# Performance work log

Measured on AMD Instinct MI355X. Metric: run time of the kernel, lower is better.

## Reference

```python
import jax, jax.numpy as jnp
import numpy as np

B, N, DIM, HEADS, DIM_HEAD = 1, 8192, 512, 8, 64  # dim == heads*dim_head required by pos_emb
EPS = 1e-12  # F.normalize eps


def setup_inputs() -> dict:
    key = jax.random.key(0)
    ks = jax.random.split(key, 13)
    w = lambda k, shape: jax.random.normal(k, shape, dtype=jnp.float32) * 0.02
    return {
        "x_in": jax.random.normal(ks[0], (B, N, DIM), dtype=jnp.float32),
        "task_x": jax.random.normal(ks[1], (B, N, DIM), dtype=jnp.float32),
        "Ges": jax.random.uniform(ks[2], (1, 1, N, N), dtype=jnp.float32) / N,  # OT transport plan (precomputed constant)
        "Wq": w(ks[3], (DIM, DIM)),
        "Wk": w(ks[4], (DIM, DIM)),
        "Wv": w(ks[5], (DIM, DIM)),
        "rescale": jnp.ones((HEADS, 1, 1), dtype=jnp.float32),
        "Wp": w(ks[6], (DIM, DIM)),
        "bp": jnp.zeros((DIM,), dtype=jnp.float32),
        "W1": w(ks[7], (DIM, DIM)),
        "b1": jnp.zeros((DIM,), dtype=jnp.float32),
        "W2": w(ks[8], (DIM, DIM)),
        "b2": jnp.zeros((DIM,), dtype=jnp.float32),
    }


def _l2norm(x):
    # F.normalize(p=2, dim=-1): x / max(||x||, eps)
    n = jnp.sqrt(jnp.sum(x * x, axis=-1, keepdims=True))
    return x / jnp.maximum(n, EPS)


def reference(x_in, task_x, Ges, Wq, Wk, Wv, rescale, Wp, bp, W1, b1, W2, b2):
    b, n, c = x_in.shape
    q_inp = x_in @ Wq.T          # [b,n,hd]
    k_inp = x_in @ Wk.T
    v_inp = x_in @ Wv.T
    split = lambda t: t.reshape(b, n, HEADS, DIM_HEAD).transpose(0, 2, 1, 3)  # [b,h,n,d]
    q, k, v, tx = split(q_inp), split(k_inp), split(v_inp), split(task_x)
    guided = (Ges @ tx) * v       # [b,h,n,d]: OT-guided embedding multiply
    # channel attention: operate along n, attend over d
    qT = _l2norm(q.transpose(0, 1, 3, 2))   # [b,h,d,n]
    kT = _l2norm(k.transpose(0, 1, 3, 2))   # [b,h,d,n]
    gT = guided.transpose(0, 1, 3, 2)        # [b,h,d,n]
    attn = jnp.einsum('bhdn,bhen->bhde', kT, qT) * rescale  # [b,h,d,d]
    attn = jax.nn.softmax(attn, axis=-1)
    x = attn @ gT                 # [b,h,d,n]
    x = x.transpose(0, 3, 1, 2).reshape(b, n, HEADS * DIM_HEAD)  # [b,n,hd]
    out_c = x @ Wp.T + bp
    out_p = (jax.nn.gelu(v_inp @ W1.T + b1, approximate=False)) @ W2.T + b2
    return out_c + out_p
```

## Files before the change

kernel.cpp:

```cpp
#include <hip/hip_runtime.h>
#include <hip/hip_bf16.h>

typedef unsigned short u16;
typedef __attribute__((ext_vector_type(8))) short short8v;
typedef __attribute__((ext_vector_type(4))) float f32x4;

typedef __attribute__((address_space(3))) char lds_char;
typedef const __attribute__((address_space(1))) char g_char;

__device__ __forceinline__ u16 f2bf(float f) {
    union { float f; unsigned int u; } x; x.f = f;
    unsigned int u = x.u;
    return (u16)((u + 0x7FFFu + ((u >> 16) & 1u)) >> 16);
}
__device__ __forceinline__ float bf2f(u16 h) {
    union { unsigned int u; float f; } x; x.u = ((unsigned int)h) << 16;
    return x.f;
}
__device__ __forceinline__ u16 cvtbf(float f) {
    return __builtin_bit_cast(u16, __float2bfloat16(f));
}
__device__ __forceinline__ void gload16(const void* g, void* l) {
    __builtin_amdgcn_global_load_lds((g_char*)g, (lds_char*)l, 16, 0, 0);
}

template<int EPI, bool AF32>
__global__ __launch_bounds__(256, 3) void gemm_k(
    const void* __restrict__ Ap, int lda,
    const u16* __restrict__ Bt, int ldb,
    void* __restrict__ Cp, int ldc, int K)
{
    constexpr int ATB = AF32 ? 32768 : 16384;
    __shared__ alignas(16) char smem[ATB + 16384];

    const int t     = threadIdx.x;
    const int lane  = t & 63;
    const int wid   = t >> 6;
    const int m0    = blockIdx.x * 128;
    const int n0    = blockIdx.y * 128;
    const int kbase = blockIdx.z * K;
    const int wr    = wid >> 1, wc = wid & 1;
    const int lr    = lane & 15, q4 = lane >> 4;

    f32x4 acc[4][4];
    #pragma unroll
    for (int i = 0; i < 4; ++i)
        #pragma unroll
        for (int j = 0; j < 4; ++j)
            acc[i][j] = (f32x4){0.f, 0.f, 0.f, 0.f};

    const int nsteps = K >> 6;
    for (int kt = 0; kt < nsteps; ++kt) {
        const int k0 = kbase + (kt << 6);
        if constexpr (AF32) {
            const float* A32 = (const float*)Ap;
            #pragma unroll
            for (int p = 0; p < 8; ++p) {
                int o   = p * 4096 + t * 16;
                int row = o >> 8;
                int cb  = (o & 255) ^ ((row & 15) << 4);
                gload16(A32 + (size_t)(m0 + row) * (size_t)lda + k0 + (cb >> 2),
                        smem + o);
            }
        } else {
            const u16* A16 = (const u16*)Ap;
            #pragma unroll
            for (int p = 0; p < 4; ++p) {
                int o   = p * 4096 + t * 16;
                int row = o >> 7;
                int cb  = (o & 127) ^ ((row & 7) << 4);
                gload16(A16 + (size_t)(m0 + row) * (size_t)lda + k0 + (cb >> 1),
                        smem + o);
            }
        }
        #pragma unroll
        for (int p = 0; p < 4; ++p) {
            int o   = p * 4096 + t * 16;
            int row = o >> 7;
            int cb  = (o & 127) ^ ((row & 7) << 4);
            gload16(Bt + (size_t)(n0 + row) * (size_t)ldb + k0 + (cb >> 1),
                    smem + ATB + o);
        }
        __syncthreads();

        #pragma unroll
        for (int kh = 0; kh < 2; ++kh) {
            short8v a[4], b[4];
            #pragma unroll
            for (int i = 0; i < 4; ++i) {
                int ar = wr * 64 + i * 16 + lr;
                if constexpr (AF32) {
                    int cb0 = kh * 128 + q4 * 32;
                    int sw  = (ar & 15) << 4;
                    f32x4 f0 = *(const f32x4*)(smem + ar * 256 + (cb0 ^ sw));
                    f32x4 f1 = *(const f32x4*)(smem + ar * 256 + ((cb0 + 16) ^ sw));
                    short8v av;
                    #pragma unroll
                    for (int j = 0; j < 4; ++j) {
                        av[j]     = (short)cvtbf(f0[j]);
                        av[j + 4] = (short)cvtbf(f1[j]);
                    }
                    a[i] = av;
                } else {
                    a[i] = *(const short8v*)(smem + ar * 128 +
                            ((kh * 64 + q4 * 16) ^ ((ar & 7) << 4)));
                }
            }
            #pragma unroll
            for (int i = 0; i < 4; ++i) {
                int br = wc * 64 + i * 16 + lr;
                b[i] = *(const short8v*)(smem + ATB + br * 128 +
                        ((kh * 64 + q4 * 16) ^ ((br & 7) << 4)));
            }
            #pragma unroll
            for (int mi = 0; mi < 4; ++mi)
                #pragma unroll
                for (int ni = 0; ni < 4; ++ni)
                    acc[mi][ni] = __builtin_amdgcn_mfma_f32_16x16x32_bf16(
                        a[mi], b[ni], acc[mi][ni], 0, 0, 0);
        }
        __syncthreads();
    }

    const size_t zoff = (size_t)blockIdx.z * 8192ull * (size_t)ldc;
    #pragma unroll
    for (int mi = 0; mi < 4; ++mi) {
        #pragma unroll
        for (int ni = 0; ni < 4; ++ni) {
            const int gc = n0 + wc * 64 + ni * 16 + lr;
            #pragma unroll
            for (int j = 0; j < 4; ++j) {
                const int gr = m0 + wr * 64 + mi * 16 + q4 * 4 + j;
                float v = acc[mi][ni][j];
                if constexpr (EPI == 0) {
                    ((u16*)Cp)[(size_t)gr * ldc + gc] = f2bf(v);
                } else {
                    ((float*)Cp)[zoff + (size_t)gr * ldc + gc] = v;
                }
            }
        }
    }
}

template<int KZ, int MODE>
__global__ void k_cmb(const float* __restrict__ P, const u16* __restrict__ QKV,
                      const float* __restrict__ bvec, void* __restrict__ dst)
{
    for (int i = blockIdx.x * 256 + threadIdx.x; i < 1048576;
         i += gridDim.x * 256) {
        const int r = i >> 7, c = (i & 127) * 4;
        f32x4 s = ((const f32x4*)P)[i];
        #pragma unroll
        for (int z = 1; z < KZ; ++z) {
            f32x4 q = ((const f32x4*)P)[(size_t)z * 1048576 + i];
            s[0] += q[0]; s[1] += q[1]; s[2] += q[2]; s[3] += q[3];
        }
        if constexpr (MODE == 1) {
            ushort4 v = *(const ushort4*)(QKV + (size_t)r * 1536 + 1024 + c);
            ushort4 o;
            o.x = cvtbf(s[0] * bf2f(v.x)); o.y = cvtbf(s[1] * bf2f(v.y));
            o.z = cvtbf(s[2] * bf2f(v.z)); o.w = cvtbf(s[3] * bf2f(v.w));
            *(ushort4*)((u16*)dst + (size_t)r * 1024 + c) = o;
        } else if constexpr (MODE == 2) {
            float4 b = *(const float4*)(bvec + c);
            float x0 = s[0] + b.x, x1 = s[1] + b.y, x2 = s[2] + b.z, x3 = s[3] + b.w;
            ushort4 o;
            o.x = cvtbf(0.5f * x0 * (1.0f + erff(x0 * 0.70710678118f)));
            o.y = cvtbf(0.5f * x1 * (1.0f + erff(x1 * 0.70710678118f)));
            o.z = cvtbf(0.5f * x2 * (1.0f + erff(x2 * 0.70710678118f)));
            o.w = cvtbf(0.5f * x3 * (1.0f + erff(x3 * 0.70710678118f)));
            *(ushort4*)((u16*)dst + (size_t)r * 1024 + 512 + c) = o;
        } else {
            float4 b = *(const float4*)(bvec + c);
            float4 o = {s[0] + b.x, s[1] + b.y, s[2] + b.z, s[3] + b.w};
            *(float4*)((float*)dst + (size_t)r * 512 + c) = o;
        }
    }
}

__global__ void k_convert(const float* __restrict__ Wq, const float* __restrict__ Wk,
                          const float* __restrict__ Wv, const float* __restrict__ W1,
                          u16* __restrict__ WqkvB, u16* __restrict__ W1B)
{
    const int C2 = 196608;
    const int C3 = 65536;
    for (int i = blockIdx.x * blockDim.x + threadIdx.x; i < C2 + C3;
         i += gridDim.x * blockDim.x) {
        const float* src; u16* dst;
        if (i < C2) {
            int e = i * 4;
            if (e < 262144)      src = Wq + e;
            else if (e < 524288) src = Wk + (e - 262144);
            else                 src = Wv + (e - 524288);
            dst = WqkvB + e;
        } else {
            int e = (i - C2) * 4;
            src = W1 + e; dst = W1B + e;
        }
        float4 v = *reinterpret_cast<const float4*>(src);
        ushort4 h;
        h.x = f2bf(v.x); h.y = f2bf(v.y); h.z = f2bf(v.z); h.w = f2bf(v.w);
        *reinterpret_cast<ushort4*>(dst) = h;
    }
}

__global__ void k_transpose(const float* __restrict__ tx, u16* __restrict__ txt)
{
    __shared__ float tile[64][65];
    const int n0 = blockIdx.x * 64;
    const int c0 = blockIdx.y * 64;
    const int t = threadIdx.x;
    #pragma unroll
    for (int p = 0; p < 4; ++p) {
        int q = p * 256 + t;
        int r = q >> 4, s = q & 15;
        float4 v = *reinterpret_cast<const float4*>(tx + (size_t)(n0 + r) * 512 + c0 + s * 4);
        tile[r][s * 4 + 0] = v.x; tile[r][s * 4 + 1] = v.y;
        tile[r][s * 4 + 2] = v.z; tile[r][s * 4 + 3] = v.w;
    }
    __syncthreads();
    #pragma unroll
    for (int p = 0; p < 4; ++p) {
        int q = p * 256 + t;
        int cc = q >> 4, s = q & 15;
        ushort4 h;
        h.x = f2bf(tile[s * 4 + 0][cc]); h.y = f2bf(tile[s * 4 + 1][cc]);
        h.z = f2bf(tile[s * 4 + 2][cc]); h.w = f2bf(tile[s * 4 + 3][cc]);
        *reinterpret_cast<ushort4*>(txt + (size_t)(c0 + cc) * 8192 + n0 + s * 4) = h;
    }
}

__global__ void k_colsq(const u16* __restrict__ QKV, float* __restrict__ colsq)
{
    const int t = threadIdx.x;
    const int c8 = t & 127, rs = t >> 7;
    float a[8];
    #pragma unroll
    for (int j = 0; j < 8; ++j) a[j] = 0.f;
    const int row0 = blockIdx.x * 64;
    for (int rr = rs; rr < 64; rr += 2) {
        uint4 u = *reinterpret_cast<const uint4*>(QKV + (size_t)(row0 + rr) * 1536 + c8 * 8);
        unsigned int w[4] = {u.x, u.y, u.z, u.w};
        #pragma unroll
        for (int q = 0; q < 4; ++q) {
            float f0 = bf2f((u16)(w[q] & 0xffffu));
            float f1 = bf2f((u16)(w[q] >> 16));
            a[2 * q]     += f0 * f0;
            a[2 * q + 1] += f1 * f1;
        }
    }
    #pragma unroll
    for (int j = 0; j < 8; ++j) atomicAdd(&colsq[c8 * 8 + j], a[j]);
}

__global__ void k_gram(const u16* __restrict__ QKV, float* __restrict__ Sb)
{
    __shared__ u16 Qt[4][64];
    __shared__ u16 Kt[4][64];
    const int h = blockIdx.x >> 6;
    const int chunk = blockIdx.x & 63;
    const int t = threadIdx.x;
    const int e = t & 63;
    const int dg = t >> 6;
    float acc[16];
    #pragma unroll
    for (int k = 0; k < 16; ++k) acc[k] = 0.f;
    const int rowbase = chunk * 128;
    for (int p = 0; p < 32; ++p) {
        __syncthreads();
        if (t < 64) {
            const int mat = t >> 5, sub = t & 31, r = sub >> 3, seg = sub & 7;
            const int row = rowbase + p * 4 + r;
            const int col = (mat ? 512 : 0) + h * 64 + seg * 8;
            uint4 v = *reinterpret_cast<const uint4*>(QKV + (size_t)row * 1536 + col);
            u16* dst = mat ? &Kt[r][seg * 8] : &Qt[r][seg * 8];
            *reinterpret_cast<uint4*>(dst) = v;
        }
        __syncthreads();
        #pragma unroll
        for (int r = 0; r < 4; ++r) {
            const float q = bf2f(Qt[r][e]);
            short8v kv0 = *reinterpret_cast<const short8v*>(&Kt[r][dg * 16]);
            short8v kv1 = *reinterpret_cast<const short8v*>(&Kt[r][dg * 16 + 8]);
            #pragma unroll
            for (int k = 0; k < 8; ++k) {
                acc[k]     += bf2f((u16)kv0[k]) * q;
                acc[k + 8] += bf2f((u16)kv1[k]) * q;
            }
        }
    }
    #pragma unroll
    for (int k = 0; k < 16; ++k)
        atomicAdd(&Sb[h * 4096 + (dg * 16 + k) * 64 + e], acc[k]);
}

__global__ void k_softmax(const float* __restrict__ Sb, const float* __restrict__ colsq,
                          const float* __restrict__ rescale, float* __restrict__ Abuf)
{
    const int h = blockIdx.x;
    const int t = threadIdx.x;
    const float rsc = rescale[h];
    const float nq = fmaxf(sqrtf(colsq[h * 64 + t]), 1e-12f);
    for (int d = 0; d < 64; ++d) {
        const float nk = fmaxf(sqrtf(colsq[512 + h * 64 + d]), 1e-12f);
        float v = Sb[h * 4096 + d * 64 + t] / (nk * nq) * rsc;
        float m = v;
        #pragma unroll
        for (int off = 32; off > 0; off >>= 1) m = fmaxf(m, __shfl_xor(m, off, 64));
        float p = expf(v - m);
        float s = p;
        #pragma unroll
        for (int off = 32; off > 0; off >>= 1) s += __shfl_xor(s, off, 64);
        Abuf[h * 4096 + d * 64 + t] = p / s;
    }
}

__global__ void k_buildbt(const float* __restrict__ Abuf, const float* __restrict__ Wp,
                          const float* __restrict__ W2, const float* __restrict__ bp,
                          const float* __restrict__ b2, u16* __restrict__ BtC,
                          float* __restrict__ bsum)
{
    const int g = blockIdx.x * 256 + threadIdx.x;
    const int j = g >> 10, c = g & 1023;
    if (c < 512) {
        const int h = c >> 6, e = c & 63;
        const float* Ah = Abuf + h * 4096 + e;
        const float* Wph = Wp + (size_t)j * 512 + h * 64;
        float s = 0.f;
        #pragma unroll 8
        for (int d = 0; d < 64; ++d) s += Ah[d * 64] * Wph[d];
        BtC[(size_t)j * 1024 + c] = f2bf(s);
        if (c == 0) bsum[j] = bp[j] + b2[j];
    } else {
        BtC[(size_t)j * 1024 + c] = f2bf(W2[(size_t)j * 512 + (c - 512)]);
    }
}

extern "C" void kernel_launch(void* const* d_in, const int* in_sizes, int n_in,
                              void* d_out, int out_size, void* d_ws, size_t ws_size,
                              hipStream_t stream)
{
    const float* x_in    = (const float*)d_in[0];
    const float* task_x  = (const float*)d_in[1];
    const float* Ges     = (const float*)d_in[2];
    const float* Wq      = (const float*)d_in[3];
    const float* Wk      = (const float*)d_in[4];
    const float* Wv      = (const float*)d_in[5];
    const float* rescale = (const float*)d_in[6];
    const float* Wp      = (const float*)d_in[7];
    const float* bp      = (const float*)d_in[8];
    const float* W1      = (const float*)d_in[9];
    const float* b1      = (const float*)d_in[10];
    const float* W2      = (const float*)d_in[11];
    const float* b2      = (const float*)d_in[12];
    float* out = (float*)d_out;
    char* ws = (char*)d_ws;

    u16*   TXT   = (u16*)  (ws + 0);
    u16*   QKV   = (u16*)  (ws + 8388608);
    u16*   AH    = (u16*)  (ws + 33554432);
    u16*   WqkvB = (u16*)  (ws + 50331648);
    u16*   W1B   = (u16*)  (ws + 51904512);
    u16*   BtC   = (u16*)  (ws + 52428800);
    float* colsq = (float*)(ws + 53477376);
    float* Sb    = (float*)(ws + 53481472);
    float* Abuf  = (float*)(ws + 53612544);
    float* bsum  = (float*)(ws + 53743616);
    float* P     = (float*)(ws + 53745664);
    (void)in_sizes; (void)n_in; (void)out_size; (void)ws_size;

    hipMemsetAsync(colsq, 0, 135168, stream);

    k_convert  <<<512, 256, 0, stream>>>(Wq, Wk, Wv, W1, WqkvB, W1B);
    k_transpose<<<dim3(128, 8), 256, 0, stream>>>(task_x, TXT);

    gemm_k<0, true><<<dim3(64, 12, 1), 256, 0, stream>>>(
        x_in, 512, WqkvB, 512, QKV, 1536, 512);

    k_colsq  <<<128, 256, 0, stream>>>(QKV, colsq);
    k_gram   <<<512, 256, 0, stream>>>(QKV, Sb);
    k_softmax<<<8, 64, 0, stream>>>(Sb, colsq, rescale, Abuf);
    k_buildbt<<<2048, 256, 0, stream>>>(Abuf, Wp, W2, bp, b2, BtC, bsum);

    gemm_k<4, true><<<dim3(64, 4, 4), 256, 0, stream>>>(
        Ges, 8192, TXT, 8192, P, 512, 2048);
    k_cmb<4, 1><<<1024, 256, 0, stream>>>(P, QKV, nullptr, AH);

    gemm_k<4, false><<<dim3(64, 4, 2), 256, 0, stream>>>(
        QKV + 1024, 1536, W1B, 512, P, 512, 256);
    k_cmb<2, 2><<<1024, 256, 0, stream>>>(P, nullptr, b1, AH);

    gemm_k<4, false><<<dim3(64, 4, 2), 256, 0, stream>>>(
        AH, 1024, BtC, 1024, P, 512, 512);
    k_cmb<2, 3><<<1024, 256, 0, stream>>>(P, nullptr, bsum, out);
}
```

Baseline: 369.7 us.

## Convert fp32 A tiles to bf16 before LDS store; widen gram staging tile

In the GEMM, fp32 A tiles are now loaded into registers, converted to bf16 once and written to LDS. The old path staged fp32 through async global-to-LDS loads and converted on every fragment read. This halves the A tile's LDS footprint (allowing better occupancy) and removes repeated conversions, at the cost of synchronous register-staged loads that no longer bypass VGPRs. In the gram kernel, each iteration now stages 16 rows with all threads instead of 4 rows with 64 threads, cutting the number of barriers per block.

```diff
diff --git a/kernel.cpp b/kernel.cpp
--- a/kernel.cpp
+++ b/kernel.cpp
@@ -30,8 +30,7 @@
     const u16* __restrict__ Bt, int ldb,
     void* __restrict__ Cp, int ldc, int K)
 {
-    constexpr int ATB = AF32 ? 32768 : 16384;
-    __shared__ alignas(16) char smem[ATB + 16384];
+    __shared__ alignas(16) char smem[32768];
 
     const int t     = threadIdx.x;
     const int lane  = t & 63;
@@ -52,15 +51,18 @@
     const int nsteps = K >> 6;
     for (int kt = 0; kt < nsteps; ++kt) {
         const int k0 = kbase + (kt << 6);
+
+        float4 ar[8];
         if constexpr (AF32) {
             const float* A32 = (const float*)Ap;
             #pragma unroll
-            for (int p = 0; p < 8; ++p) {
+            for (int p = 0; p < 4; ++p) {
                 int o   = p * 4096 + t * 16;
-                int row = o >> 8;
-                int cb  = (o & 255) ^ ((row & 15) << 4);
-                gload16(A32 + (size_t)(m0 + row) * (size_t)lda + k0 + (cb >> 2),
-                        smem + o);
+                int row = o >> 7;
+                int fc  = (o & 127) >> 1;
+                const float* gp = A32 + (size_t)(m0 + row) * (size_t)lda + k0 + fc;
+                ar[2 * p]     = *(const float4*)gp;
+                ar[2 * p + 1] = *(const float4*)(gp + 4);
             }
         } else {
             const u16* A16 = (const u16*)Ap;
@@ -79,7 +81,23 @@
             int row = o >> 7;
             int cb  = (o & 127) ^ ((row & 7) << 4);
             gload16(Bt + (size_t)(n0 + row) * (size_t)ldb + k0 + (cb >> 1),
-                    smem + ATB + o);
+                    smem + 16384 + o);
+        }
+        if constexpr (AF32) {
+            #pragma unroll
+            for (int p = 0; p < 4; ++p) {
+                int o   = p * 4096 + t * 16;
+                int row = o >> 7;
+                int cb  = o & 127;
+                const float* f0 = (const float*)&ar[2 * p];
+                const float* f1 = (const float*)&ar[2 * p + 1];
+                uint4 w;
+                w.x = (unsigned)cvtbf(f0[0]) | ((unsigned)cvtbf(f0[1]) << 16);
+                w.y = (unsigned)cvtbf(f0[2]) | ((unsigned)cvtbf(f0[3]) << 16);
+                w.z = (unsigned)cvtbf(f1[0]) | ((unsigned)cvtbf(f1[1]) << 16);
+                w.w = (unsigned)cvtbf(f1[2]) | ((unsigned)cvtbf(f1[3]) << 16);
+                *(uint4*)(smem + row * 128 + (cb ^ ((row & 7) << 4))) = w;
+            }
         }
         __syncthreads();
 
@@ -88,28 +106,14 @@
             short8v a[4], b[4];
             #pragma unroll
             for (int i = 0; i < 4; ++i) {
-                int ar = wr * 64 + i * 16 + lr;
-                if constexpr (AF32) {
-                    int cb0 = kh * 128 + q4 * 32;
-                    int sw  = (ar & 15) << 4;
-                    f32x4 f0 = *(const f32x4*)(smem + ar * 256 + (cb0 ^ sw));
-                    f32x4 f1 = *(const f32x4*)(smem + ar * 256 + ((cb0 + 16) ^ sw));
-                    short8v av;
-                    #pragma unroll
-                    for (int j = 0; j < 4; ++j) {
-                        av[j]     = (short)cvtbf(f0[j]);
-                        av[j + 4] = (short)cvtbf(f1[j]);
-                    }
-                    a[i] = av;
-                } else {
-                    a[i] = *(const short8v*)(smem + ar * 128 +
-                            ((kh * 64 + q4 * 16) ^ ((ar & 7) << 4)));
-                }
+                int arr = wr * 64 + i * 16 + lr;
+                a[i] = *(const short8v*)(smem + arr * 128 +
+                        ((kh * 64 + q4 * 16) ^ ((arr & 7) << 4)));
             }
             #pragma unroll
             for (int i = 0; i < 4; ++i) {
                 int br = wc * 64 + i * 16 + lr;
-                b[i] = *(const short8v*)(smem + ATB + br * 128 +
+                b[i] = *(const short8v*)(smem + 16384 + br * 128 +
                         ((kh * 64 + q4 * 16) ^ ((br & 7) << 4)));
             }
             #pragma unroll
@@ -255,8 +259,8 @@
 
 __global__ void k_gram(const u16* __restrict__ QKV, float* __restrict__ Sb)
 {
-    __shared__ u16 Qt[4][64];
-    __shared__ u16 Kt[4][64];
+    __shared__ u16 Qt[16][64];
+    __shared__ u16 Kt[16][64];
     const int h = blockIdx.x >> 6;
     const int chunk = blockIdx.x & 63;
     const int t = threadIdx.x;
@@ -266,11 +270,11 @@
     #pragma unroll
     for (int k = 0; k < 16; ++k) acc[k] = 0.f;
     const int rowbase = chunk * 128;
-    for (int p = 0; p < 32; ++p) {
+    for (int p = 0; p < 8; ++p) {
         __syncthreads();
-        if (t < 64) {
-            const int mat = t >> 5, sub = t & 31, r = sub >> 3, seg = sub & 7;
-            const int row = rowbase + p * 4 + r;
+        {
+            const int mat = t >> 7, sub = t & 127, r = sub >> 3, seg = sub & 7;
+            const int row = rowbase + p * 16 + r;
             const int col = (mat ? 512 : 0) + h * 64 + seg * 8;
             uint4 v = *reinterpret_cast<const uint4*>(QKV + (size_t)row * 1536 + col);
             u16* dst = mat ? &Kt[r][seg * 8] : &Qt[r][seg * 8];
@@ -278,7 +282,7 @@
         }
         __syncthreads();
         #pragma unroll
-        for (int r = 0; r < 4; ++r) {
+        for (int r = 0; r < 16; ++r) {
             const float q = bf2f(Qt[r][e]);
             short8v kv0 = *reinterpret_cast<const short8v*>(&Kt[r][dg * 16]);
             short8v kv1 = *reinterpret_cast<const short8v*>(&Kt[r][dg * 16 + 8]);
```

Result: slower. 429.3 us (+16.1%).

## Pre-convert Ges and x_in to bf16 and simplify GEMM to bf16-only A

Applied to the files above, without the earlier changes.

Adds a standalone kernel that converts the large Ges matrix to bf16 and extends the weight-conversion kernel to also convert x_in. The GEMM kernel drops its fp32-A path, halving its LDS footprint and raising the occupancy hint. This removes per-tile fp32 loads and in-loop conversions. In exchange, it adds an extra full pass writing and then re-reading a bf16 copy of Ges each call.

```diff
diff --git a/kernel.cpp b/kernel.cpp
--- a/kernel.cpp
+++ b/kernel.cpp
@@ -24,14 +24,13 @@
     __builtin_amdgcn_global_load_lds((g_char*)g, (lds_char*)l, 16, 0, 0);
 }
 
-template<int EPI, bool AF32>
-__global__ __launch_bounds__(256, 3) void gemm_k(
-    const void* __restrict__ Ap, int lda,
+template<int EPI>
+__global__ __launch_bounds__(256, 4) void gemm_k(
+    const u16* __restrict__ Ab, int lda,
     const u16* __restrict__ Bt, int ldb,
     void* __restrict__ Cp, int ldc, int K)
 {
-    constexpr int ATB = AF32 ? 32768 : 16384;
-    __shared__ alignas(16) char smem[ATB + 16384];
+    __shared__ alignas(16) char smem[32768];
 
     const int t     = threadIdx.x;
     const int lane  = t & 63;
@@ -52,26 +51,13 @@
     const int nsteps = K >> 6;
     for (int kt = 0; kt < nsteps; ++kt) {
         const int k0 = kbase + (kt << 6);
-        if constexpr (AF32) {
-            const float* A32 = (const float*)Ap;
-            #pragma unroll
-            for (int p = 0; p < 8; ++p) {
-                int o   = p * 4096 + t * 16;
-                int row = o >> 8;
-                int cb  = (o & 255) ^ ((row & 15) << 4);
-                gload16(A32 + (size_t)(m0 + row) * (size_t)lda + k0 + (cb >> 2),
-                        smem + o);
-            }
-        } else {
-            const u16* A16 = (const u16*)Ap;
-            #pragma unroll
-            for (int p = 0; p < 4; ++p) {
-                int o   = p * 4096 + t * 16;
-                int row = o >> 7;
-                int cb  = (o & 127) ^ ((row & 7) << 4);
-                gload16(A16 + (size_t)(m0 + row) * (size_t)lda + k0 + (cb >> 1),
-                        smem + o);
-            }
+        #pragma unroll
+        for (int p = 0; p < 4; ++p) {
+            int o   = p * 4096 + t * 16;
+            int row = o >> 7;
+            int cb  = (o & 127) ^ ((row & 7) << 4);
+            gload16(Ab + (size_t)(m0 + row) * (size_t)lda + k0 + (cb >> 1),
+                    smem + o);
         }
         #pragma unroll
         for (int p = 0; p < 4; ++p) {
@@ -79,7 +65,7 @@
             int row = o >> 7;
             int cb  = (o & 127) ^ ((row & 7) << 4);
             gload16(Bt + (size_t)(n0 + row) * (size_t)ldb + k0 + (cb >> 1),
-                    smem + ATB + o);
+                    smem + 16384 + o);
         }
         __syncthreads();
 
@@ -89,27 +75,13 @@
             #pragma unroll
             for (int i = 0; i < 4; ++i) {
                 int ar = wr * 64 + i * 16 + lr;
-                if constexpr (AF32) {
-                    int cb0 = kh * 128 + q4 * 32;
-                    int sw  = (ar & 15) << 4;
-                    f32x4 f0 = *(const f32x4*)(smem + ar * 256 + (cb0 ^ sw));
-                    f32x4 f1 = *(const f32x4*)(smem + ar * 256 + ((cb0 + 16) ^ sw));
-                    short8v av;
-                    #pragma unroll
-                    for (int j = 0; j < 4; ++j) {
-                        av[j]     = (short)cvtbf(f0[j]);
-                        av[j + 4] = (short)cvtbf(f1[j]);
-                    }
-                    a[i] = av;
-                } else {
-                    a[i] = *(const short8v*)(smem + ar * 128 +
-                            ((kh * 64 + q4 * 16) ^ ((ar & 7) << 4)));
-                }
+                a[i] = *(const short8v*)(smem + ar * 128 +
+                        ((kh * 64 + q4 * 16) ^ ((ar & 7) << 4)));
             }
             #pragma unroll
             for (int i = 0; i < 4; ++i) {
                 int br = wc * 64 + i * 16 + lr;
-                b[i] = *(const short8v*)(smem + ATB + br * 128 +
+                b[i] = *(const short8v*)(smem + 16384 + br * 128 +
                         ((kh * 64 + q4 * 16) ^ ((br & 7) << 4)));
             }
             #pragma unroll
@@ -178,23 +150,43 @@
     }
 }
 
-__global__ void k_convert(const float* __restrict__ Wq, const float* __restrict__ Wk,
+__global__ void k_cges(const float* __restrict__ g, u16* __restrict__ gb)
+{
+    const int total = 8388608;
+    for (int i = blockIdx.x * 256 + threadIdx.x; i < total;
+         i += gridDim.x * 256) {
+        const float4* s = (const float4*)(g + (size_t)i * 8);
+        float4 a = s[0], b = s[1];
+        uint4 o;
+        o.x = (unsigned)cvtbf(a.x) | ((unsigned)cvtbf(a.y) << 16);
+        o.y = (unsigned)cvtbf(a.z) | ((unsigned)cvtbf(a.w) << 16);
+        o.z = (unsigned)cvtbf(b.x) | ((unsigned)cvtbf(b.y) << 16);
+        o.w = (unsigned)cvtbf(b.z) | ((unsigned)cvtbf(b.w) << 16);
+        *(uint4*)(gb + (size_t)i * 8) = o;
+    }
+}
+
+__global__ void k_convert(const float* __restrict__ x_in,
+                          const float* __restrict__ Wq, const float* __restrict__ Wk,
                           const float* __restrict__ Wv, const float* __restrict__ W1,
-                          u16* __restrict__ WqkvB, u16* __restrict__ W1B)
-{
+                          u16* __restrict__ XB, u16* __restrict__ WqkvB,
+                          u16* __restrict__ W1B)
+{
+    const int C1 = 1048576;
     const int C2 = 196608;
     const int C3 = 65536;
-    for (int i = blockIdx.x * blockDim.x + threadIdx.x; i < C2 + C3;
+    for (int i = blockIdx.x * blockDim.x + threadIdx.x; i < C1 + C2 + C3;
          i += gridDim.x * blockDim.x) {
         const float* src; u16* dst;
-        if (i < C2) {
-            int e = i * 4;
+        if (i < C1) { src = x_in + (size_t)i * 4; dst = XB + (size_t)i * 4; }
+        else if (i < C1 + C2) {
+            int e = (i - C1) * 4;
             if (e < 262144)      src = Wq + e;
             else if (e < 524288) src = Wk + (e - 262144);
             else                 src = Wv + (e - 524288);
             dst = WqkvB + e;
         } else {
-            int e = (i - C2) * 4;
+            int e = (i - C1 - C2) * 4;
             src = W1 + e; dst = W1B + e;
         }
         float4 v = *reinterpret_cast<const float4*>(src);
@@ -356,41 +348,44 @@
     float* out = (float*)d_out;
     char* ws = (char*)d_ws;
 
-    u16*   TXT   = (u16*)  (ws + 0);
-    u16*   QKV   = (u16*)  (ws + 8388608);
-    u16*   AH    = (u16*)  (ws + 33554432);
-    u16*   WqkvB = (u16*)  (ws + 50331648);
-    u16*   W1B   = (u16*)  (ws + 51904512);
-    u16*   BtC   = (u16*)  (ws + 52428800);
-    float* colsq = (float*)(ws + 53477376);
-    float* Sb    = (float*)(ws + 53481472);
-    float* Abuf  = (float*)(ws + 53612544);
-    float* bsum  = (float*)(ws + 53743616);
-    float* P     = (float*)(ws + 53745664);
+    u16*   XB    = (u16*)  (ws + 0);
+    u16*   TXT   = (u16*)  (ws + 8388608);
+    u16*   QKV   = (u16*)  (ws + 16777216);
+    u16*   AH    = (u16*)  (ws + 41943040);
+    u16*   WqkvB = (u16*)  (ws + 58720256);
+    u16*   W1B   = (u16*)  (ws + 60293120);
+    u16*   BtC   = (u16*)  (ws + 60817408);
+    float* colsq = (float*)(ws + 61865984);
+    float* Sb    = (float*)(ws + 61870080);
+    float* Abuf  = (float*)(ws + 62001152);
+    float* bsum  = (float*)(ws + 62132224);
+    float* P     = (float*)(ws + 62134272);
+    u16*   GesB  = (u16*)  (ws + 129243136);
     (void)in_sizes; (void)n_in; (void)out_size; (void)ws_size;
 
     hipMemsetAsync(colsq, 0, 135168, stream);
 
-    k_convert  <<<512, 256, 0, stream>>>(Wq, Wk, Wv, W1, WqkvB, W1B);
+    k_convert  <<<2048, 256, 0, stream>>>(x_in, Wq, Wk, Wv, W1, XB, WqkvB, W1B);
     k_transpose<<<dim3(128, 8), 256, 0, stream>>>(task_x, TXT);
-
-    gemm_k<0, true><<<dim3(64, 12, 1), 256, 0, stream>>>(
-        x_in, 512, WqkvB, 512, QKV, 1536, 512);
+    k_cges     <<<2048, 256, 0, stream>>>(Ges, GesB);
+
+    gemm_k<0><<<dim3(64, 12, 1), 256, 0, stream>>>(
+        XB, 512, WqkvB, 512, QKV, 1536, 512);
 
     k_colsq  <<<128, 256, 0, stream>>>(QKV, colsq);
     k_gram   <<<512, 256, 0, stream>>>(QKV, Sb);
     k_softmax<<<8, 64, 0, stream>>>(Sb, colsq, rescale, Abuf);
     k_buildbt<<<2048, 256, 0, stream>>>(Abuf, Wp, W2, bp, b2, BtC, bsum);
 
-    gemm_k<4, true><<<dim3(64, 4, 4), 256, 0, stream>>>(
-        Ges, 8192, TXT, 8192, P, 512, 2048);
+    gemm_k<4><<<dim3(64, 4, 4), 256, 0, stream>>>(
+        GesB, 8192, TXT, 8192, P, 512, 2048);
     k_cmb<4, 1><<<1024, 256, 0, stream>>>(P, QKV, nullptr, AH);
 
-    gemm_k<4, false><<<dim3(64, 4, 2), 256, 0, stream>>>(
+    gemm_k<4><<<dim3(64, 4, 2), 256, 0, stream>>>(
         QKV + 1024, 1536, W1B, 512, P, 512, 256);
     k_cmb<2, 2><<<1024, 256, 0, stream>>>(P, nullptr, b1, AH);
 
-    gemm_k<4, false><<<dim3(64, 4, 2), 256, 0, stream>>>(
+    gemm_k<4><<<dim3(64, 4, 2), 256, 0, stream>>>(
         AH, 1024, BtC, 1024, P, 512, 512);
     k_cmb<2, 3><<<1024, 256, 0, stream>>>(P, nullptr, bsum, out);
 }
```

New measurement: 417.1 us. +12.8%, slower.
